# Performance work log

Measured on AMD Instinct MI355X. Metric: run time of the kernel, lower is better.

Reference implementation:

```python
import jax, jax.numpy as jnp
import numpy as np

T = 1048576      # signal length
K = 3            # number of IMFs
ALPHA = 2000.0   # bandwidth penalty
TAU = 1e-7       # dual ascent step
TOL = 1e-6       # convergence tolerance
N_ITER = 50      # max fixed-point iterations


def _vmd(x, omega_init):
    T_ = x.shape[0]
    t = jnp.arange(1, T_ + 1, dtype=jnp.float32) / T_
    freqs = t - 0.5 - 1.0 / T_                           # [T]
    f_hat = jnp.fft.fftshift(jnp.fft.fft(x))             # [T] complex
    u0 = jnp.zeros((K, T_), dtype=f_hat.dtype)
    lam0 = jnp.zeros((T_,), dtype=f_hat.dtype)

    def step(carry, n):
        u_prev, lam_prev, omega, done = carry
        base = (freqs[None, :] - omega[:, None]) ** 2    # [K,T]
        # mode k's denom also gets (freqs-omega[k-1])^2 and (freqs-omega[k+1])^2
        nbr = jnp.zeros_like(base).at[1:].add(base[:-1]).at[:-1].add(base[1:])
        denom = base + nbr + TAU ** 2
        u_hat = (f_hat[None, :] - lam_prev[None, :] / 2.0) / (1.0 + ALPHA * denom)
        pw = jnp.real(u_hat) ** 2 + jnp.imag(u_hat) ** 2  # |u_hat|^2, [K,T]
        omega_new = jnp.sum(freqs[None, :] * pw, axis=1) / jnp.sum(pw, axis=1)
        lam_new = lam_prev + TAU * (jnp.sum(u_hat, axis=0) - f_hat)
        # convergence check (every 10th iter), mirrors the original break
        u_diff = jnp.sum(jnp.abs(u_hat - u_prev) ** 2) / jnp.sum(jnp.abs(u_prev) ** 2)
        om_diff = jnp.sum(jnp.abs(omega_new - jnp.roll(omega_new, 1))) / K
        conv = (n % 10 == 0) & (u_diff < TOL) & (om_diff < TOL)
        # freeze state once converged (break-iteration's fresh u_hat is kept)
        u_out = jnp.where(done, u_prev, u_hat)
        lam_out = jnp.where(done, lam_prev, lam_new)
        om_out = jnp.where(done, omega, omega_new)
        return (u_out, lam_out, om_out, done | conv), None

    init = (u0, lam0, omega_init.astype(jnp.float32), jnp.array(False))
    (u_hat, _, _, _), _ = jax.lax.scan(jax.checkpoint(step), init, jnp.arange(N_ITER))
    imfs = jnp.real(jnp.fft.ifft(jnp.fft.ifftshift(u_hat, axes=-1), axis=-1))
    return imfs.astype(jnp.float32)                      # [K,T]


def setup_inputs() -> dict:
    key = jax.random.key(0)
    kx, ko = jax.random.split(key)
    x = jax.random.normal(kx, (T,), dtype=jnp.float32)
    omega_init = jax.random.uniform(ko, (K,), dtype=jnp.float32) * 0.5  # init==1
    return {"x": x, "omega_init": omega_init}


def reference(x, omega_init):
    return _vmd(x, omega_init)
```

## Files before the change

### kernel.cpp

```cpp
#include <hip/hip_runtime.h>
#include <math.h>


#define ALPHA_F 2000.0f
#define TAU_F   1e-7f

static __device__ __forceinline__ int lpad2(int i) { return i + (i >> 4); }
static __device__ __forceinline__ int swz(int i)  { return ((i & 7) << 7) | (i >> 3); }
static __device__ __forceinline__ int swzA(int i) { return ((i & 7) << 6) | (i >> 3); }
static __device__ __forceinline__ float frcp(float x) { return __builtin_amdgcn_rcpf(x); }

typedef float v2f __attribute__((ext_vector_type(2)));
static __device__ __forceinline__ v2f sp(float s) { v2f r; r.x = s; r.y = s; return r; }
static __device__ __forceinline__ v2f v2(float a, float b) { v2f r; r.x = a; r.y = b; return r; }
static __device__ __forceinline__ v2f pkfma(v2f a, v2f b, v2f c)
{ return __builtin_elementwise_fma(a, b, c); }
static __device__ __forceinline__ v2f cmul(v2f a, v2f w)
{
  v2f t = a * sp(w.x);
  v2f s = v2(-a.y, a.x);
  return pkfma(s, sp(w.y), t);
}
static __device__ __forceinline__ v2f cmulrr(v2f a, float wr, float wi)
{
  v2f t = a * sp(wr);
  v2f s = v2(-a.y, a.x);
  return pkfma(s, sp(wi), t);
}

#define PADN2 1088

template<int CTRL>
static __device__ __forceinline__ float dpp_addf(float v)
{
  int r = __builtin_amdgcn_update_dpp(0, __float_as_int(v), CTRL, 0xf, 0xf, true);
  return v + __int_as_float(r);
}
static __device__ __forceinline__ float wave64_sum(float v)
{
  v = dpp_addf<0x111>(v);
  v = dpp_addf<0x112>(v);
  v = dpp_addf<0x114>(v);
  v = dpp_addf<0x118>(v);
  v = dpp_addf<0x142>(v);
  v = dpp_addf<0x143>(v);
  return v;
}
static __device__ __forceinline__ float row8_sum(float v)
{
  v = dpp_addf<0x111>(v);
  v = dpp_addf<0x112>(v);
  v = dpp_addf<0x114>(v);
  return v;
}
static __device__ __forceinline__ float rdlane(float v, int l)
{
  return __int_as_float(__builtin_amdgcn_readlane(__float_as_int(v), l));
}

template<int SIGN>
static __device__ __forceinline__ void bfly4(v2f Y0, v2f Y1, v2f Y2, v2f Y3,
    float w1r, float w1i, float w2r, float w2i, float w3r, float w3i,
    v2f& o0, v2f& o1, v2f& o2, v2f& o3)
{
  v2f y1 = cmulrr(Y1, w1r, w1i), y2 = cmulrr(Y2, w2r, w2i),
      y3 = cmulrr(Y3, w3r, w3i);
  v2f t0 = Y0 + y2, t1 = Y0 - y2, t2 = y1 + y3, t3 = y1 - y3;
  o0 = t0 + t2; o2 = t0 - t2;
  v2f ns3 = v2(t3.y, -t3.x);
  if (SIGN < 0) { o1 = t1 + ns3; o3 = t1 - ns3; }
  else          { o1 = t1 - ns3; o3 = t1 + ns3; }
}
template<int SIGN>
static __device__ __forceinline__ void bfly4_nt(v2f X0, v2f X1, v2f X2, v2f X3,
    v2f& o0, v2f& o1, v2f& o2, v2f& o3)
{
  v2f t0 = X0 + X2, t1 = X0 - X2, t2 = X1 + X3, t3 = X1 - X3;
  o0 = t0 + t2; o2 = t0 - t2;
  v2f ns3 = v2(t3.y, -t3.x);
  if (SIGN < 0) { o1 = t1 + ns3; o3 = t1 - ns3; }
  else          { o1 = t1 - ns3; o3 = t1 + ns3; }
}

template<int SIGN>
static __device__ void fft1024p_reg(v2f X0, v2f X1, v2f X2, v2f X3,
                                    v2f* A, v2f* B)
{
  const int u = threadIdx.x;
  {
    v2f o0, o1, o2, o3;
    bfly4_nt<SIGN>(X0, X1, X2, X3, o0, o1, o2, o3);
    const int base = u << 2;
    B[lpad2(base    )] = o0; B[lpad2(base + 1)] = o1;
    B[lpad2(base + 2)] = o2; B[lpad2(base + 3)] = o3;
    __syncthreads();
  }
#pragma unroll
  for (int st = 1; st < 5; ++st) {
    v2f *in  = (st & 1) ? B : A;
    v2f *out = (st & 1) ? A : B;
    const int quarter = 1 << (2 * st);
    const int p = u & (quarter - 1);
    const int g = u >> (2 * st);

    float sw, cw;
    sincospif((float)(2 * p) * (1.0f / (float)(4 << (2 * st))), &sw, &cw);
    const float w1r = cw, w1i = (SIGN < 0) ? -sw : sw;
    const float w2r = w1r * w1r - w1i * w1i, w2i = 2.0f * w1r * w1i;
    const float w3r = w2r * w1r - w2i * w1i, w3i = w2r * w1i + w2i * w1r;

    v2f o0, o1, o2, o3;
    bfly4<SIGN>(in[lpad2(u)], in[lpad2(u + 256)],
                in[lpad2(u + 512)], in[lpad2(u + 768)],
                w1r, w1i, w2r, w2i, w3r, w3i, o0, o1, o2, o3);

    const int base = (g << (2 * st + 2)) + p;
    out[lpad2(base              )] = o0;
    out[lpad2(base +     quarter)] = o1;
    out[lpad2(base + 2 * quarter)] = o2;
    out[lpad2(base + 3 * quarter)] = o3;
    __syncthreads();
  }
}

template<int SIGN>
static __device__ void fft1024p_dual(const v2f X[4], const v2f Y[4],
                                     v2f* A1, v2f* B1, v2f* A2, v2f* B2)
{
  const int u = threadIdx.x;
  {
    v2f o0, o1, o2, o3, p0, p1, p2, p3;
    bfly4_nt<SIGN>(X[0], X[1], X[2], X[3], o0, o1, o2, o3);
    bfly4_nt<SIGN>(Y[0], Y[1], Y[2], Y[3], p0, p1, p2, p3);
    const int base = u << 2;
    B1[lpad2(base    )] = o0; B1[lpad2(base + 1)] = o1;
    B1[lpad2(base + 2)] = o2; B1[lpad2(base + 3)] = o3;
    B2[lpad2(base    )] = p0; B2[lpad2(base + 1)] = p1;
    B2[lpad2(base + 2)] = p2; B2[lpad2(base + 3)] = p3;
    __syncthreads();
  }
#pragma unroll
  for (int st = 1; st < 5; ++st) {
    v2f *in1  = (st & 1) ? B1 : A1, *out1 = (st & 1) ? A1 : B1;
    v2f *in2  = (st & 1) ? B2 : A2, *out2 = (st & 1) ? A2 : B2;
    const int quarter = 1 << (2 * st);
    const int p = u & (quarter - 1);
    const int g = u >> (2 * st);

    float sw, cw;
    sincospif((float)(2 * p) * (1.0f / (float)(4 << (2 * st))), &sw, &cw);
    const float w1r = cw, w1i = (SIGN < 0) ? -sw : sw;
    const float w2r = w1r * w1r - w1i * w1i, w2i = 2.0f * w1r * w1i;
    const float w3r = w2r * w1r - w2i * w1i, w3i = w2r * w1i + w2i * w1r;

    v2f o0, o1, o2, o3, p0, p1, p2, p3;
    bfly4<SIGN>(in1[lpad2(u)], in1[lpad2(u + 256)],
                in1[lpad2(u + 512)], in1[lpad2(u + 768)],
                w1r, w1i, w2r, w2i, w3r, w3i, o0, o1, o2, o3);
    bfly4<SIGN>(in2[lpad2(u)], in2[lpad2(u + 256)],
                in2[lpad2(u + 512)], in2[lpad2(u + 768)],
                w1r, w1i, w2r, w2i, w3r, w3i, p0, p1, p2, p3);

    const int base = (g << (2 * st + 2)) + p;
    out1[lpad2(base              )] = o0;
    out1[lpad2(base +     quarter)] = o1;
    out1[lpad2(base + 2 * quarter)] = o2;
    out1[lpad2(base + 3 * quarter)] = o3;
    out2[lpad2(base              )] = p0;
    out2[lpad2(base +     quarter)] = p1;
    out2[lpad2(base + 2 * quarter)] = p2;
    out2[lpad2(base + 3 * quarter)] = p3;
    __syncthreads();
  }
}

__global__ __launch_bounds__(256) void k_fwd_passA(const float* __restrict__ x,
                                                   float2* __restrict__ ws0)
{
  __shared__ __align__(16) v2f A[PADN2], B[PADN2];
  const int p = swzA(blockIdx.x);
  const int tid = threadIdx.x;
  const int c0 = 2 * p;
  v2f X[4];
#pragma unroll
  for (int q = 0; q < 4; ++q)
    X[q] = ((const v2f*)x)[(size_t)(tid + 256 * q) * 512 + p];
  fft1024p_reg<-1>(X[0], X[1], X[2], X[3], A, B);

  float sa, ca, sb, cb, ssa, cca, ssb, ccb;
  sincospif((float)(c0 * tid) * (2.0f / 1048576.0f), &sa, &ca);
  sincospif((float)((c0 + 1) * tid) * (2.0f / 1048576.0f), &sb, &cb);
  sincospif((float)c0 * (1.0f / 2048.0f), &ssa, &cca);
  sincospif((float)(c0 + 1) * (1.0f / 2048.0f), &ssb, &ccb);
  v2f E0 = v2(ca, -sa), E1 = v2(cb, -sb);
  const v2f S0 = v2(cca, -ssa), S1 = v2(ccb, -ssb);
#pragma unroll
  for (int q = 0; q < 4; ++q) {
    int k = tid + 256 * q;
    int kk = (1024 - k) & 1023;
    v2f Z = B[lpad2(k)];
    v2f Wv = B[lpad2(kk)];
    float X0r = 0.5f * (Z.x + Wv.x), X0i = 0.5f * (Z.y - Wv.y);
    float X1r = 0.5f * (Z.y + Wv.y), X1i = 0.5f * (Wv.x - Z.x);
    v2f o01 = cmul(v2(X0r, X0i), E0);
    v2f o23 = cmul(v2(X1r, X1i), E1);
    if (k <= 512) {
      float4 o = make_float4(o01.x, o01.y, o23.x, o23.y);
      ((float4*)ws0)[(size_t)k * 512 + p] = o;
    }
    E0 = cmul(E0, S0); E1 = cmul(E1, S1);
  }
}

__global__ __launch_bounds__(256) void k_fwd_passB(const float2* __restrict__ ws0,
                                                   float2* __restrict__ fhat,
                                                   float* __restrict__ ET)
{
  __shared__ __align__(16) v2f A[PADN2], B[PADN2];
  const int b = blockIdx.x;
  const int tid = threadIdx.x;
  v2f X[4];
#pragma unroll
  for (int q = 0; q < 4; ++q)
    X[q] = ((const v2f*)ws0)[(size_t)b * 1024 + tid + 256 * q];
  fft1024p_reg<-1>(X[0], X[1], X[2], X[3], A, B);
  const bool mir = (b >= 1) && (b <= 511);
#pragma unroll
  for (int q = 0; q < 4; ++q) {
    int k2 = tid + 256 * q;
    v2f v = B[lpad2(k2)];
    float e = v.x * v.x + v.y * v.y;
    fhat[(size_t)b * 1024 + k2] = make_float2(v.x, v.y);
    ET[(size_t)k2 * 1024 + b] = e;
    if (mir) {
      fhat[(size_t)(1024 - b) * 1024 + (1023 - k2)] = make_float2(v.x, -v.y);
      ET[(size_t)(1023 - k2) * 1024 + (1024 - b)] = e;
    }
  }
}

static __device__ __forceinline__ void lag4(float x, float& l0, float& l1,
                                            float& l2, float& l3)
{
  float m0 = x, m1 = x - (1.0f / 3.0f), m2 = x - (2.0f / 3.0f), m3 = x - 1.0f;
  l0 = -4.5f * m1 * m2 * m3;
  l1 = 13.5f * m0 * m2 * m3;
  l2 = -13.5f * m0 * m1 * m3;
  l3 =  4.5f * m0 * m1 * m2;
}

__global__ __launch_bounds__(256) void k_moments(const float* __restrict__ ET,
                                                 double* __restrict__ W)
{
  __shared__ double red[4 * 4];
  const int B = blockIdx.x;
  const int k2 = B ^ 512;
  const int tid = threadIdx.x;
  double a0 = 0, a1 = 0, a2 = 0, a3 = 0;
#pragma unroll
  for (int q = 0; q < 4; ++q) {
    int k1 = tid + 256 * q;
    float e = ET[(size_t)k2 * 1024 + k1];
    float l0, l1, l2, l3;
    lag4((float)k1 * (1.0f / 1024.0f), l0, l1, l2, l3);
    a0 += (double)(e * l0); a1 += (double)(e * l1);
    a2 += (double)(e * l2); a3 += (double)(e * l3);
  }
  const int lane = tid & 63, wv = tid >> 6;
  double pv[4] = { a0, a1, a2, a3 };
#pragma unroll
  for (int j = 0; j < 4; ++j) {
    double v = pv[j];
    for (int off = 32; off; off >>= 1) v += __shfl_down(v, off, 64);
    if (lane == 0) red[wv * 4 + j] = v;
  }
  __syncthreads();
  if (tid < 4)
    W[B * 4 + tid] = red[tid] + red[4 + tid] + red[8 + tid] + red[12 + tid];
}

__global__ __launch_bounds__(512) void k_solve(
    const double* __restrict__ W4, const float* __restrict__ omega_init,
    float* __restrict__ ckeepN, float* __restrict__ omegaF)
{
  __shared__ float red[2][64];
  const int t = threadIdx.x;
  const int lane = t & 63, wv = t >> 6;

  float Wsc[8], fsc[8];
#pragma unroll
  for (int e = 0; e < 8; ++e) {
    Wsc[e] = (float)W4[t * 8 + e];
    int bin = 2 * t + (e >> 2);
    fsc[e] = (float)((double)bin / 1024.0 + (double)(e & 3) / 3072.0 - 0.5);
  }
  v2f frA[4], WrA[4], WfA[4], cnA[4];
#pragma unroll
  for (int i = 0; i < 4; ++i) {
    frA[i] = v2(fsc[2 * i], fsc[2 * i + 1]);
    WrA[i] = v2(Wsc[2 * i], Wsc[2 * i + 1]);
    WfA[i] = WrA[i] * frA[i];
    cnA[i] = sp(0.0f);
  }
  float om0 = omega_init[0], om1 = omega_init[1], om2 = omega_init[2];

#pragma unroll 1
  for (int it = 0; it < 49; ++it) {
    float* rb = red[it & 1];
    v2f p0 = sp(0.f), p1 = sp(0.f), p2 = sp(0.f),
        p3 = sp(0.f), p4 = sp(0.f), p5 = sp(0.f);

#pragma unroll
    for (int i = 0; i < 4; ++i) {
      const v2f fv = frA[i];
      v2f a0 = fv - sp(om0), a1 = fv - sp(om1), a2 = fv - sp(om2);
      v2f d0 = a0 * a0, d1 = a1 * a1, d2 = a2 * a2;
      v2f s01 = d0 + d1, s12 = d1 + d2;
      v2f dA = pkfma(sp(ALPHA_F), s01, sp(1.0f));
      v2f dC = pkfma(sp(ALPHA_F), s12, sp(1.0f));
      v2f dB = pkfma(sp(ALPHA_F), d2, dA);
      v2f AB = dA * dB, BC = dB * dC, AC = dA * dC;
      v2f ABC = AB * dC;
      float rr = frcp(ABC.x * ABC.y);
      v2f r = v2(rr * ABC.y, rr * ABC.x);
      v2f w0 = BC * r, w1 = AC * r, w2 = AB * r;
      v2f hf = pkfma(sp(-0.5f), cnA[i], sp(1.0f));
      v2f g = hf * hf;
      v2f gw0 = g * (w0 * w0), gw1 = g * (w1 * w1), gw2 = g * (w2 * w2);
      p0 = pkfma(WfA[i], gw0, p0); p1 = pkfma(WfA[i], gw1, p1);
      p2 = pkfma(WfA[i], gw2, p2);
      p3 = pkfma(WrA[i], gw0, p3); p4 = pkfma(WrA[i], gw1, p4);
      p5 = pkfma(WrA[i], gw2, p5);
      v2f S = (w0 + w1) + w2;
      cnA[i] = pkfma(sp(TAU_F), pkfma(S, hf, sp(-1.0f)), cnA[i]);
    }

    float q0 = p0.x + p0.y, q1 = p1.x + p1.y, q2 = p2.x + p2.y;
    float q3 = p3.x + p3.y, q4 = p4.x + p4.y, q5 = p5.x + p5.y;

    q0 = wave64_sum(q0); q1 = wave64_sum(q1); q2 = wave64_sum(q2);
    q3 = wave64_sum(q3); q4 = wave64_sum(q4); q5 = wave64_sum(q5);
    if (lane == 63) {
      rb[0 * 8 + wv] = q0; rb[1 * 8 + wv] = q1; rb[2 * 8 + wv] = q2;
      rb[3 * 8 + wv] = q3; rb[4 * 8 + wv] = q4; rb[5 * 8 + wv] = q5;
    }
    __syncthreads();
    float v1 = rb[lane];
    v1 = row8_sum(v1);
    float n0 = rdlane(v1, 7),  n1 = rdlane(v1, 15), n2 = rdlane(v1, 23);
    float e0 = rdlane(v1, 31), e1 = rdlane(v1, 39), e2 = rdlane(v1, 47);
    om0 = n0 * frcp(e0);
    om1 = n1 * frcp(e1);
    om2 = n2 * frcp(e2);
  }

  ((float4*)ckeepN)[2 * t]     = make_float4(cnA[0].x, cnA[0].y, cnA[1].x, cnA[1].y);
  ((float4*)ckeepN)[2 * t + 1] = make_float4(cnA[2].x, cnA[2].y, cnA[3].x, cnA[3].y);
  if (t == 0) { omegaF[0] = om0; omegaF[1] = om1; omegaF[2] = om2; }
}

__global__ __launch_bounds__(256) void k_inv_A2(
    const float2* __restrict__ fhat, const float* __restrict__ ckeepN,
    const float* __restrict__ omegaF, float2* __restrict__ ws0)
{
  __shared__ __align__(16) v2f A1[PADN2], B1[PADN2], A2[PADN2], B2[PADN2];
  const int tid = threadIdx.x;
  const int b = swz(blockIdx.x);
  const bool dual = (b <= 512);
  const float om0 = omegaF[0], om1 = omegaF[1], om2 = omegaF[2];
  const float xb = (float)b * (1.0f / 1024.0f);
  float l0, l1, l2, l3, m0, m1, m2, m3;
  lag4(xb, l0, l1, l2, l3);
  lag4(1.0f - xb, m0, m1, m2, m3);
  const float4* cN = (const float4*)ckeepN;

  v2f X[4];
  v2f Y[4];
#pragma unroll
  for (int q = 0; q < 4; ++q) {
    int j = tid + 256 * q;
    float2 f = fhat[(size_t)b * 1024 + j];
    int bin = j ^ 512;
    int binp = 1023 - bin;
    float4 cv = cN[bin];
    float4 cw = cN[binp];
    float c  = l0 * cv.x + l1 * cv.y + l2 * cv.z + l3 * cv.w;
    float cp = m0 * cw.x + m1 * cw.y + m2 * cw.z + m3 * cw.w;
    float hf = 1.0f - 0.5f * c;
    float hp = 1.0f - 0.5f * cp;
    int tt = (bin << 10) | b;
    float freq = (float)tt * (1.0f / 1048576.0f) - 0.5f;
    v2f fpm = v2(freq, -freq);
    v2f A0 = fpm - sp(om0), A1v = fpm - sp(om1), A2v = fpm - sp(om2);
    v2f D0 = A0 * A0, D1 = A1v * A1v, D2 = A2v * A2v;
    v2f DA = pkfma(sp(ALPHA_F), D0 + D1, sp(1.0f));
    v2f DB = pkfma(sp(ALPHA_F), D2, DA);
    float r0 = hf * frcp(DA.x), r0n = hp * frcp(DA.y);
    float r1 = hf * frcp(DB.x), r1n = hp * frcp(DB.y);
    float Rr = 0.5f * (r0 + r0n), Ri = 0.5f * (r1 + r1n);
    X[q] = cmul(v2(f.x, f.y), v2(Rr, Ri));
    if (dual) {
      v2f DC = pkfma(sp(ALPHA_F), D1 + D2, sp(1.0f));
      float r2 = hf * frcp(DC.x), r2n = hp * frcp(DC.y);
      float Rr2 = 0.5f * (r2 + r2n);
      Y[q] = v2(f.x, f.y) * sp(Rr2);
    }
  }

  float sa, ca, ss, cs;
  sincospif((float)(b * tid) * (2.0f / 1048576.0f), &sa, &ca);
  sincospif((float)b * (1.0f / 2048.0f), &ss, &cs);
  v2f E = v2(ca, sa);
  const v2f S = v2(cs, ss);

  if (dual) {
    fft1024p_dual<1>(X, Y, A1, B1, A2, B2);
    const bool mir = (b >= 1) && (b <= 511);
#pragma unroll
    for (int q = 0; q < 4; ++q) {
      int m1i = tid + 256 * q;
      v2f va = B1[lpad2(m1i)];
      v2f vb = B2[lpad2(m1i)];
      v2f oa = cmul(va, E);
      v2f ob = cmul(vb, E);
      ws0[(size_t)m1i * 1024 + b]           = make_float2(oa.x, oa.y);
      ws0[1048576 + (size_t)m1i * 1024 + b] = make_float2(ob.x, ob.y);
      if (mir)
        ws0[1048576 + (size_t)m1i * 1024 + (1024 - b)] = make_float2(ob.x, -ob.y);
      E = cmul(E, S);
    }
  } else {
    fft1024p_reg<1>(X[0], X[1], X[2], X[3], A1, B1);
#pragma unroll
    for (int q = 0; q < 4; ++q) {
      int m1i = tid + 256 * q;
      v2f va = B1[lpad2(m1i)];
      v2f oa = cmul(va, E);
      ws0[(size_t)m1i * 1024 + b] = make_float2(oa.x, oa.y);
      E = cmul(E, S);
    }
  }
}

__global__ __launch_bounds__(256) void k_inv_B2(const float2* __restrict__ ws0,
                                                float* __restrict__ out)
{
  __shared__ __align__(16) v2f A[PADN2], B[PADN2];
  const int tid = threadIdx.x;
  const float sc = 1.0f / 1048576.0f;

  if (blockIdx.x < 1024) {
    const int b = swz(blockIdx.x);
    v2f X[4];
#pragma unroll
    for (int q = 0; q < 4; ++q)
      X[q] = ((const v2f*)ws0)[(size_t)b * 1024 + tid + 256 * q];
    fft1024p_reg<1>(X[0], X[1], X[2], X[3], A, B);
#pragma unroll
    for (int q = 0; q < 4; ++q) {
      int m2 = tid + 256 * q;
      v2f v = B[lpad2(m2)];
      out[(size_t)m2 * 1024 + b]           = v.x * sc;
      out[1048576 + (size_t)m2 * 1024 + b] = v.y * sc;
    }
  } else {
    const int s = swzA(blockIdx.x - 1024);
    const int b0 = 2 * s, b1 = 2 * s + 1;
#pragma unroll
    for (int q = 0; q < 4; ++q) {
      int j = tid + 256 * q;
      A[lpad2(j)] = ((const v2f*)ws0)[1048576 + (size_t)b0 * 1024 + j];
      B[lpad2(j)] = ((const v2f*)ws0)[1048576 + (size_t)b1 * 1024 + j];
    }
    __syncthreads();
    v2f Z[4];
#pragma unroll
    for (int q = 0; q < 4; ++q) {
      int j = tid + 256 * q;
      int mj = (1024 - j) & 1023;
      v2f W0j = A[lpad2(j)], W0m = A[lpad2(mj)];
      v2f W1j = B[lpad2(j)], W1m = B[lpad2(mj)];
      float H0r = 0.5f * (W0j.x + W0m.x), H0i = 0.5f * (W0j.y - W0m.y);
      float H1r = 0.5f * (W1j.x + W1m.x), H1i = 0.5f * (W1j.y - W1m.y);
      Z[q] = v2(H0r - H1i, H0i + H1r);
    }
    __syncthreads();
    fft1024p_reg<1>(Z[0], Z[1], Z[2], Z[3], A, B);
#pragma unroll
    for (int q = 0; q < 4; ++q) {
      int m2 = tid + 256 * q;
      v2f v = B[lpad2(m2)];
      out[2097152 + (size_t)m2 * 1024 + b0] = v.x * sc;
      out[2097152 + (size_t)m2 * 1024 + b1] = v.y * sc;
    }
  }
}

extern "C" void kernel_launch(void* const* d_in, const int* in_sizes, int n_in,
                              void* d_out, int out_size, void* d_ws, size_t ws_size,
                              hipStream_t stream)
{
  (void)in_sizes; (void)n_in; (void)out_size; (void)ws_size;
  const float* x       = (const float*)d_in[0];
  const float* om_init = (const float*)d_in[1];
  float* out = (float*)d_out;

  char* w = (char*)d_ws;
  const size_t MB = 1024ull * 1024ull;
  float2* fhat     = (float2*)(w);
  float*  ET       = (float*)(w + 8 * MB);
  double* W4       = (double*)(w + 12 * MB);
  float*  ckeepN   = (float*)(w + 12 * MB + 32 * 1024);
  float*  omegaF   = (float*)(w + 12 * MB + 48 * 1024);
  float2* scratch  = (float2*)(w + 16 * MB);

  k_fwd_passA<<<512, 256, 0, stream>>>(x, scratch);
  k_fwd_passB<<<513, 256, 0, stream>>>(scratch, fhat, ET);
  k_moments<<<1024, 256, 0, stream>>>(ET, W4);
  k_solve<<<1, 512, 0, stream>>>(W4, om_init, ckeepN, omegaF);
  k_inv_A2<<<1024, 256, 0, stream>>>(fhat, ckeepN, omegaF, scratch);
  k_inv_B2<<<1536, 256, 0, stream>>>(scratch, out);
}
```

Measured before the change: 172.7 us.

## Trim solver math, split solve into two launches, special-case Nyquist output in passA

The forward passA epilogue now loops over two quarters instead of four and writes the k=512 Nyquist bin from a single thread using its own twiddle. This removes the wasted iterations that previously skipped their stores. The serial k_solve loop is algebraically reworked: the squared denominators are folded into FMAs, hf is folded into the reciprocal weights, and two reciprocals are shared. The 49 iterations are now split across two launches (25 and 24), with state saved to and reloaded from global memory, which adds a launch and may change floating-point rounding.

```diff
diff --git a/kernel.cpp b/kernel.cpp
--- a/kernel.cpp
+++ b/kernel.cpp
@@ -195,7 +195,7 @@
   v2f E0 = v2(ca, -sa), E1 = v2(cb, -sb);
   const v2f S0 = v2(cca, -ssa), S1 = v2(ccb, -ssb);
 #pragma unroll
-  for (int q = 0; q < 4; ++q) {
+  for (int q = 0; q < 2; ++q) {
     int k = tid + 256 * q;
     int kk = (1024 - k) & 1023;
     v2f Z = B[lpad2(k)];
@@ -204,11 +204,19 @@
     float X1r = 0.5f * (Z.y + Wv.y), X1i = 0.5f * (Wv.x - Z.x);
     v2f o01 = cmul(v2(X0r, X0i), E0);
     v2f o23 = cmul(v2(X1r, X1i), E1);
-    if (k <= 512) {
-      float4 o = make_float4(o01.x, o01.y, o23.x, o23.y);
-      ((float4*)ws0)[(size_t)k * 512 + p] = o;
-    }
-    E0 = cmul(E0, S0); E1 = cmul(E1, S1);
+    float4 o = make_float4(o01.x, o01.y, o23.x, o23.y);
+    ((float4*)ws0)[(size_t)k * 512 + p] = o;
+    if (q == 0) { E0 = cmul(E0, S0); E1 = cmul(E1, S1); }
+  }
+  if (tid == 0) {
+    v2f Z = B[lpad2(512)];
+    float s0, c0f, s1, c1f;
+    sincospif((float)c0 * (1.0f / 1024.0f), &s0, &c0f);
+    sincospif((float)(c0 + 1) * (1.0f / 1024.0f), &s1, &c1f);
+    v2f o01 = cmul(v2(Z.x, 0.0f), v2(c0f, -s0));
+    v2f o23 = cmul(v2(Z.y, 0.0f), v2(c1f, -s1));
+    float4 o = make_float4(o01.x, o01.y, o23.x, o23.y);
+    ((float4*)ws0)[(size_t)512 * 512 + p] = o;
   }
 }
 
@@ -281,7 +289,8 @@
 
 __global__ __launch_bounds__(512) void k_solve(
     const double* __restrict__ W4, const float* __restrict__ omega_init,
-    float* __restrict__ ckeepN, float* __restrict__ omegaF)
+    float* __restrict__ ckeepN, float* __restrict__ omegaF,
+    int nit, int load)
 {
   __shared__ float red[2][64];
   const int t = threadIdx.x;
@@ -302,10 +311,19 @@
     WfA[i] = WrA[i] * frA[i];
     cnA[i] = sp(0.0f);
   }
-  float om0 = omega_init[0], om1 = omega_init[1], om2 = omega_init[2];
+  float om0, om1, om2;
+  if (load) {
+    om0 = omegaF[0]; om1 = omegaF[1]; om2 = omegaF[2];
+    float4 c0 = ((const float4*)ckeepN)[2 * t];
+    float4 c1 = ((const float4*)ckeepN)[2 * t + 1];
+    cnA[0] = v2(c0.x, c0.y); cnA[1] = v2(c0.z, c0.w);
+    cnA[2] = v2(c1.x, c1.y); cnA[3] = v2(c1.z, c1.w);
+  } else {
+    om0 = omega_init[0]; om1 = omega_init[1]; om2 = omega_init[2];
+  }
 
 #pragma unroll 1
-  for (int it = 0; it < 49; ++it) {
+  for (int it = 0; it < nit; ++it) {
     float* rb = red[it & 1];
     v2f p0 = sp(0.f), p1 = sp(0.f), p2 = sp(0.f),
         p3 = sp(0.f), p4 = sp(0.f), p5 = sp(0.f);
@@ -314,25 +332,25 @@
     for (int i = 0; i < 4; ++i) {
       const v2f fv = frA[i];
       v2f a0 = fv - sp(om0), a1 = fv - sp(om1), a2 = fv - sp(om2);
-      v2f d0 = a0 * a0, d1 = a1 * a1, d2 = a2 * a2;
-      v2f s01 = d0 + d1, s12 = d1 + d2;
-      v2f dA = pkfma(sp(ALPHA_F), s01, sp(1.0f));
-      v2f dC = pkfma(sp(ALPHA_F), s12, sp(1.0f));
-      v2f dB = pkfma(sp(ALPHA_F), d2, dA);
+      v2f t0 = sp(ALPHA_F) * a0, t1 = sp(ALPHA_F) * a1, t2 = sp(ALPHA_F) * a2;
+      v2f m1 = pkfma(t1, a1, sp(1.0f));
+      v2f dA = pkfma(t0, a0, m1);
+      v2f dC = pkfma(t2, a2, m1);
+      v2f dB = pkfma(t2, a2, dA);
       v2f AB = dA * dB, BC = dB * dC, AC = dA * dC;
       v2f ABC = AB * dC;
       float rr = frcp(ABC.x * ABC.y);
       v2f r = v2(rr * ABC.y, rr * ABC.x);
-      v2f w0 = BC * r, w1 = AC * r, w2 = AB * r;
       v2f hf = pkfma(sp(-0.5f), cnA[i], sp(1.0f));
-      v2f g = hf * hf;
-      v2f gw0 = g * (w0 * w0), gw1 = g * (w1 * w1), gw2 = g * (w2 * w2);
-      p0 = pkfma(WfA[i], gw0, p0); p1 = pkfma(WfA[i], gw1, p1);
-      p2 = pkfma(WfA[i], gw2, p2);
-      p3 = pkfma(WrA[i], gw0, p3); p4 = pkfma(WrA[i], gw1, p4);
-      p5 = pkfma(WrA[i], gw2, p5);
-      v2f S = (w0 + w1) + w2;
-      cnA[i] = pkfma(sp(TAU_F), pkfma(S, hf, sp(-1.0f)), cnA[i]);
+      v2f hr = hf * r;
+      v2f v0 = hr * BC, v1 = hr * AC, v2_ = hr * AB;
+      v2f g0 = v0 * v0, g1 = v1 * v1, g2 = v2_ * v2_;
+      p0 = pkfma(WfA[i], g0, p0); p1 = pkfma(WfA[i], g1, p1);
+      p2 = pkfma(WfA[i], g2, p2);
+      p3 = pkfma(WrA[i], g0, p3); p4 = pkfma(WrA[i], g1, p4);
+      p5 = pkfma(WrA[i], g2, p5);
+      v2f vs = ((v0 + v1) + v2_) - sp(1.0f);
+      cnA[i] = pkfma(sp(TAU_F), vs, cnA[i]);
     }
 
     float q0 = p0.x + p0.y, q1 = p1.x + p1.y, q2 = p2.x + p2.y;
@@ -345,12 +363,13 @@
       rb[3 * 8 + wv] = q3; rb[4 * 8 + wv] = q4; rb[5 * 8 + wv] = q5;
     }
     __syncthreads();
-    float v1 = rb[lane];
-    v1 = row8_sum(v1);
-    float n0 = rdlane(v1, 7),  n1 = rdlane(v1, 15), n2 = rdlane(v1, 23);
-    float e0 = rdlane(v1, 31), e1 = rdlane(v1, 39), e2 = rdlane(v1, 47);
-    om0 = n0 * frcp(e0);
-    om1 = n1 * frcp(e1);
+    float v1r = red[it & 1][lane];
+    v1r = row8_sum(v1r);
+    float n0 = rdlane(v1r, 7),  n1 = rdlane(v1r, 15), n2 = rdlane(v1r, 23);
+    float e0 = rdlane(v1r, 31), e1 = rdlane(v1r, 39), e2 = rdlane(v1r, 47);
+    float ie01 = frcp(e0 * e1);
+    om0 = n0 * (ie01 * e1);
+    om1 = n1 * (ie01 * e0);
     om2 = n2 * frcp(e2);
   }
 
@@ -517,7 +536,8 @@
   k_fwd_passA<<<512, 256, 0, stream>>>(x, scratch);
   k_fwd_passB<<<513, 256, 0, stream>>>(scratch, fhat, ET);
   k_moments<<<1024, 256, 0, stream>>>(ET, W4);
-  k_solve<<<1, 512, 0, stream>>>(W4, om_init, ckeepN, omegaF);
+  k_solve<<<1, 512, 0, stream>>>(W4, om_init, ckeepN, omegaF, 25, 0);
+  k_solve<<<1, 512, 0, stream>>>(W4, om_init, ckeepN, omegaF, 24, 1);
   k_inv_A2<<<1024, 256, 0, stream>>>(fhat, ckeepN, omegaF, scratch);
   k_inv_B2<<<1536, 256, 0, stream>>>(scratch, out);
 }
```

New measurement: 173.7 us. No clear change (+0.5%).
